# Performance work log

Hardware: AMD Instinct MI355X
Metric: run time of the kernel (lower is better)

The kernel has to match this reference:

```python
import jax, jax.numpy as jnp
import numpy as np

N_NODES = 100000
N_EDGES = 600000
IN_DIM = 128
HID = 128
OUT_DIM = 64
N_LAYERS = 3


def setup_inputs() -> dict:
    key = jax.random.key(0)
    ks = jax.random.split(key, 8)
    x = jax.random.normal(ks[0], (N_NODES, IN_DIM), dtype=jnp.float32)
    edge_index = jax.random.randint(ks[1], (2, N_EDGES), 0, N_NODES, dtype=jnp.int64)
    s = 1.0 / np.sqrt(HID)
    W_in = jax.random.normal(ks[2], (HID, IN_DIM), dtype=jnp.float32) * s
    b_in = jax.random.normal(ks[3], (HID,), dtype=jnp.float32) * s
    W_convs = jax.random.normal(ks[4], (N_LAYERS, HID, HID), dtype=jnp.float32) * s
    b_convs = jax.random.normal(ks[5], (N_LAYERS, HID), dtype=jnp.float32) * s
    W_out = jax.random.normal(ks[6], (OUT_DIM, (N_LAYERS + 1) * HID), dtype=jnp.float32) * s
    b_out = jax.random.normal(ks[7], (OUT_DIM,), dtype=jnp.float32) * s
    return {"x": x, "edge_index": edge_index, "W_in": W_in, "b_in": b_in,
            "W_convs": W_convs, "b_convs": b_convs, "W_out": W_out, "b_out": b_out}


def reference(x, edge_index, W_in, b_in, W_convs, b_convs, W_out, b_out):
    src, dst = edge_index[0], edge_index[1]
    n = x.shape[0]
    # input projection: [N, in] -> [N, H]
    h = x @ W_in.T + b_in
    hidden_states = [h]
    for i in range(W_convs.shape[0]):
        # GINConv (eps=0): nn(x + sum of neighbor messages), messages src->dst
        agg = jax.ops.segment_sum(h[src], dst, num_segments=n)
        h = (h + agg) @ W_convs[i].T + b_convs[i]
        hidden_states.append(h)
    cat = jnp.concatenate(hidden_states, axis=1)  # [N, (L+1)*H]
    out = cat @ W_out.T + b_out  # [N, OUT]
    return jax.nn.softmax(out, axis=-1)
```

## Files before the change

kernel.cpp:

```cpp
#include <hip/hip_runtime.h>
#include <hip/hip_bf16.h>
#include <hip/hip_fp16.h>

#define GN 100000
#define GE 600000
#define SCAN_NBLK 98

typedef __bf16    bf16x8 __attribute__((ext_vector_type(8)));
typedef __bf16    bf16x4 __attribute__((ext_vector_type(4)));
typedef _Float16  f16x8  __attribute__((ext_vector_type(8)));
typedef float     f32x4  __attribute__((ext_vector_type(4)));

__global__ __launch_bounds__(256) void convert_w(
    const float* __restrict__ Win, const float* __restrict__ Wc,
    __bf16* __restrict__ hi, __bf16* __restrict__ lo)
{
    const int i = blockIdx.x * 256 + threadIdx.x;
    if (i >= 65536) return;
    const float v = (i < 16384) ? Win[i] : Wc[i - 16384];
    const __bf16 h = (__bf16)v;
    hi[i] = h;
    lo[i] = (__bf16)(v - (float)h);
}

template<bool GATHER>
__global__ __launch_bounds__(512, 4) void gin_layer(
    const float* __restrict__ H, int ldH,
    const _Float16* __restrict__ HfIn,
    const int* __restrict__ row_start,
    const int* __restrict__ deg,
    const int* __restrict__ csr,
    const __bf16* __restrict__ Whi,
    const __bf16* __restrict__ Wlo,
    const float* __restrict__ bias,
    float* __restrict__ C, int ldC,
    _Float16* __restrict__ HfOut)
{
    constexpr int K   = 128;
    constexpr int ALD = 132;

    __shared__ float Acc[64 * ALD];

    const int tid  = threadIdx.x;
    const int wave = tid >> 6;
    const int lane = tid & 63;
    const int row0 = blockIdx.x * 64;
    const int wm   = (wave >> 2) * 32;
    const int wn   = (wave & 3) * 32;
    const int quad = lane >> 4;
    const int l15  = lane & 15;

#pragma unroll
    for (int p = 0; p < 4; ++p) {
        const int q  = tid + p * 512;
        const int r  = q >> 5;
        const int c4 = (q & 31) * 4;
        float4 v = make_float4(0.f, 0.f, 0.f, 0.f);
        if (row0 + r < GN) v = *(const float4*)(H + (size_t)(row0 + r) * ldH + c4);
        *(float4*)&Acc[r * ALD + c4] = v;
    }

    if (GATHER) {
        const uint* Hw = (const uint*)HfIn;
        float2 acc8[8];
        int start8[8], deg8[8];
        int maxd = 0;
#pragma unroll
        for (int r = 0; r < 8; ++r) {
            acc8[r] = make_float2(0.f, 0.f);
            const int v = row0 + wave * 8 + r;
            start8[r] = (v < GN) ? row_start[v] : 0;
            deg8[r]   = (v < GN) ? deg[v] : 0;
            maxd = max(maxd, deg8[r]);
        }

        int scur[8];
#pragma unroll
        for (int r = 0; r < 8; ++r) {
            const int s = csr[start8[r]];
            scur[r] = min(max(s, 0), GN - 1);
        }

        for (int k = 0; k < maxd; ++k) {
            int snext[8];
#pragma unroll
            for (int r = 0; r < 8; ++r) {
                const int kk = max(min(k + 1, deg8[r] - 1), 0);
                snext[r] = csr[start8[r] + kk];
            }
            uint t[8];
#pragma unroll
            for (int r = 0; r < 8; ++r)
                t[r] = Hw[(size_t)scur[r] * 64 + lane];
#pragma unroll
            for (int r = 0; r < 8; ++r) {
                const float m = (k < deg8[r]) ? 1.f : 0.f;
                union { uint u; _Float16 h[2]; } cv;
                cv.u = t[r];
                acc8[r].x = fmaf(m, (float)cv.h[0], acc8[r].x);
                acc8[r].y = fmaf(m, (float)cv.h[1], acc8[r].y);
                scur[r] = min(max(snext[r], 0), GN - 1);
            }
        }

        __syncthreads();
        const int j = lane * 2;
#pragma unroll
        for (int r = 0; r < 8; ++r) {
            float* a = &Acc[(wave * 8 + r) * ALD + j];
            a[0] += acc8[r].x;
            a[1] += acc8[r].y;
        }
    }
    __syncthreads();

    f32x4 acc[2][2];
#pragma unroll
    for (int i = 0; i < 2; ++i)
#pragma unroll
        for (int j = 0; j < 2; ++j) acc[i][j] = (f32x4)(0.0f);

#pragma unroll
    for (int ks = 0; ks < 4; ++ks) {
        const int kt = ks * 32 + quad * 8;
        bf16x8 ahi[2], alo[2];
#pragma unroll
        for (int mt = 0; mt < 2; ++mt) {
            const float* ap = &Acc[(wm + mt * 16 + l15) * ALD + kt];
            const f32x4 p = *(const f32x4*)ap;
            const f32x4 q = *(const f32x4*)(ap + 4);
#pragma unroll
            for (int e = 0; e < 4; ++e) {
                const __bf16 hp = (__bf16)p[e];
                const __bf16 hq = (__bf16)q[e];
                ahi[mt][e]     = hp;
                ahi[mt][e + 4] = hq;
                alo[mt][e]     = (__bf16)(p[e] - (float)hp);
                alo[mt][e + 4] = (__bf16)(q[e] - (float)hq);
            }
        }
        bf16x8 whi[2], wlo[2];
#pragma unroll
        for (int nt = 0; nt < 2; ++nt) {
            const int n = wn + nt * 16 + l15;
            whi[nt] = *(const bf16x8*)(Whi + (size_t)n * K + kt);
            wlo[nt] = *(const bf16x8*)(Wlo + (size_t)n * K + kt);
        }
#pragma unroll
        for (int mt = 0; mt < 2; ++mt)
#pragma unroll
            for (int nt = 0; nt < 2; ++nt) {
                acc[mt][nt] = __builtin_amdgcn_mfma_f32_16x16x32_bf16(
                    ahi[mt], whi[nt], acc[mt][nt], 0, 0, 0);
                acc[mt][nt] = __builtin_amdgcn_mfma_f32_16x16x32_bf16(
                    ahi[mt], wlo[nt], acc[mt][nt], 0, 0, 0);
                acc[mt][nt] = __builtin_amdgcn_mfma_f32_16x16x32_bf16(
                    alo[mt], whi[nt], acc[mt][nt], 0, 0, 0);
            }
    }
    __syncthreads();

#pragma unroll
    for (int nt = 0; nt < 2; ++nt) {
        const int col = wn + nt * 16 + l15;
        const float b = bias[col];
#pragma unroll
        for (int mt = 0; mt < 2; ++mt)
#pragma unroll
            for (int r4 = 0; r4 < 4; ++r4)
                Acc[(wm + mt * 16 + quad * 4 + r4) * ALD + col] = acc[mt][nt][r4] + b;
    }
    __syncthreads();
#pragma unroll
    for (int p = 0; p < 4; ++p) {
        const int q  = tid + p * 512;
        const int r  = q >> 5;
        const int c4 = (q & 31) * 4;
        const int gr = row0 + r;
        if (gr < GN)
            *(float4*)(C + (size_t)gr * ldC + c4) = *(const float4*)&Acc[r * ALD + c4];
    }
    if (HfOut) {
#pragma unroll
        for (int p = 0; p < 2; ++p) {
            const int q = tid + p * 512;
            const int r = q >> 4;
            const int g = (q & 15) * 8;
            const int gr = row0 + r;
            if (gr < GN) {
                const float4 a = *(const float4*)&Acc[r * ALD + g];
                const float4 b = *(const float4*)&Acc[r * ALD + g + 4];
                f16x8 o = {(_Float16)a.x, (_Float16)a.y, (_Float16)a.z, (_Float16)a.w,
                           (_Float16)b.x, (_Float16)b.y, (_Float16)b.z, (_Float16)b.w};
                *(f16x8*)&HfOut[(size_t)gr * 128 + g] = o;
            }
        }
    }
}

__global__ __launch_bounds__(512, 2) void final_gemm_softmax(
    const float* __restrict__ A,
    const float* __restrict__ Wout,
    const float* __restrict__ bias,
    float* __restrict__ out)
{
    constexpr int K   = 512;
    constexpr int ALD = 72;
    constexpr int CLD = 68;

    __shared__ char smem_raw[128 * ALD * 2 * 2];
    __bf16* Ahi = (__bf16*)smem_raw;
    __bf16* Alo = Ahi + 128 * ALD;
    float*  Cst = (float*)smem_raw;

    const int tid  = threadIdx.x;
    const int wave = tid >> 6;
    const int lane = tid & 63;
    const int row0 = blockIdx.x * 128;
    const int wm   = (wave >> 1) * 32;
    const int wn   = (wave & 1) * 32;
    const int quad = lane >> 4;
    const int l15  = lane & 15;

    f32x4 acc[2][2];
#pragma unroll
    for (int i = 0; i < 2; ++i)
#pragma unroll
        for (int j = 0; j < 2; ++j) acc[i][j] = (f32x4)(0.0f);

    for (int k0 = 0; k0 < K; k0 += 64) {
#pragma unroll
        for (int p = 0; p < 4; ++p) {
            const int q  = tid + p * 512;
            const int f  = q * 4;
            const int r  = f >> 6;
            const int kc = f & 63;
            float4 v4 = make_float4(0.f, 0.f, 0.f, 0.f);
            const int gr = row0 + r;
            if (gr < GN) v4 = *(const float4*)(A + (size_t)gr * 512 + k0 + kc);
            const __bf16 h0 = (__bf16)v4.x, h1 = (__bf16)v4.y,
                         h2 = (__bf16)v4.z, h3 = (__bf16)v4.w;
            const int idx = r * ALD + kc;
            *(bf16x4*)&Ahi[idx] = (bf16x4){h0, h1, h2, h3};
            *(bf16x4*)&Alo[idx] = (bf16x4){(__bf16)(v4.x - (float)h0),
                                           (__bf16)(v4.y - (float)h1),
                                           (__bf16)(v4.z - (float)h2),
                                           (__bf16)(v4.w - (float)h3)};
        }
        __syncthreads();

#pragma unroll
        for (int ks = 0; ks < 2; ++ks) {
            const int kt = ks * 32 + quad * 8;
            bf16x8 ahi[2], alo[2];
#pragma unroll
            for (int mt = 0; mt < 2; ++mt) {
                const int idx = (wm + mt * 16 + l15) * ALD + kt;
                ahi[mt] = *(const bf16x8*)&Ahi[idx];
                alo[mt] = *(const bf16x8*)&Alo[idx];
            }
            bf16x8 whi[2], wlo[2];
#pragma unroll
            for (int nt = 0; nt < 2; ++nt) {
                const int n = wn + nt * 16 + l15;
                const float* wp = Wout + (size_t)n * K + k0 + kt;
                const float4 p = *(const float4*)wp;
                const float4 q = *(const float4*)(wp + 4);
                float pv[8] = {p.x, p.y, p.z, p.w, q.x, q.y, q.z, q.w};
#pragma unroll
                for (int e = 0; e < 8; ++e) {
                    const __bf16 h = (__bf16)pv[e];
                    whi[nt][e] = h;
                    wlo[nt][e] = (__bf16)(pv[e] - (float)h);
                }
            }
#pragma unroll
            for (int mt = 0; mt < 2; ++mt)
#pragma unroll
                for (int nt = 0; nt < 2; ++nt) {
                    acc[mt][nt] = __builtin_amdgcn_mfma_f32_16x16x32_bf16(
                        ahi[mt], whi[nt], acc[mt][nt], 0, 0, 0);
                    acc[mt][nt] = __builtin_amdgcn_mfma_f32_16x16x32_bf16(
                        ahi[mt], wlo[nt], acc[mt][nt], 0, 0, 0);
                    acc[mt][nt] = __builtin_amdgcn_mfma_f32_16x16x32_bf16(
                        alo[mt], whi[nt], acc[mt][nt], 0, 0, 0);
                }
        }
        __syncthreads();
    }

#pragma unroll
    for (int nt = 0; nt < 2; ++nt) {
        const int col = wn + nt * 16 + l15;
        const float b = bias[col];
#pragma unroll
        for (int mt = 0; mt < 2; ++mt)
#pragma unroll
            for (int r4 = 0; r4 < 4; ++r4)
                Cst[(wm + mt * 16 + quad * 4 + r4) * CLD + col] = acc[mt][nt][r4] + b;
    }
    __syncthreads();

    for (int i = 0; i < 16; ++i) {
        const int r = wave * 16 + i;
        const float v = Cst[r * CLD + lane];
        float m = v;
#pragma unroll
        for (int off = 32; off > 0; off >>= 1) m = fmaxf(m, __shfl_xor(m, off));
        const float e = __expf(v - m);
        float s = e;
#pragma unroll
        for (int off = 32; off > 0; off >>= 1) s += __shfl_xor(s, off);
        const int gr = row0 + r;
        if (gr < GN) out[(size_t)gr * 64 + lane] = e / s;
    }
}

__global__ __launch_bounds__(256) void count_deg(const int* __restrict__ dst,
                                                 int* __restrict__ deg)
{
    const int e = blockIdx.x * 256 + threadIdx.x;
    if (e < GE) atomicAdd(&deg[dst[e]], 1);
}

__global__ __launch_bounds__(256) void scan_pass1(const int* __restrict__ deg,
                                                  int* __restrict__ excl,
                                                  int* __restrict__ blockSums)
{
    __shared__ int s[256];
    const int t = threadIdx.x;
    const int base = blockIdx.x * 1024 + t * 4;

    int4 v = make_int4(0, 0, 0, 0);
    if (base + 3 < GN) {
        v = *(const int4*)(deg + base);
    } else {
        if (base + 0 < GN) v.x = deg[base + 0];
        if (base + 1 < GN) v.y = deg[base + 1];
        if (base + 2 < GN) v.z = deg[base + 2];
        if (base + 3 < GN) v.w = deg[base + 3];
    }
    const int mysum = v.x + v.y + v.z + v.w;
    s[t] = mysum;
    __syncthreads();
    for (int off = 1; off < 256; off <<= 1) {
        const int val = (t >= off) ? s[t - off] : 0;
        __syncthreads();
        s[t] += val;
        __syncthreads();
    }
    int4 o;
    o.x = s[t] - mysum;
    o.y = o.x + v.x;
    o.z = o.y + v.y;
    o.w = o.z + v.z;
    if (base + 3 < GN) {
        *(int4*)(excl + base) = o;
    } else {
        if (base + 0 < GN) excl[base + 0] = o.x;
        if (base + 1 < GN) excl[base + 1] = o.y;
        if (base + 2 < GN) excl[base + 2] = o.z;
        if (base + 3 < GN) excl[base + 3] = o.w;
    }
    if (t == 255) blockSums[blockIdx.x] = s[255];
}

__global__ __launch_bounds__(128) void scan_pass2(const int* __restrict__ blockSums,
                                                  int* __restrict__ blockOffs, int n)
{
    __shared__ int s[128];
    const int t = threadIdx.x;
    const int v = (t < n) ? blockSums[t] : 0;
    s[t] = v;
    __syncthreads();
    for (int off = 1; off < 128; off <<= 1) {
        const int val = (t >= off) ? s[t - off] : 0;
        __syncthreads();
        s[t] += val;
        __syncthreads();
    }
    if (t < n) blockOffs[t] = s[t] - v;
}

__global__ __launch_bounds__(256) void scan_pass3(int* __restrict__ excl,
                                                  const int* __restrict__ blockOffs,
                                                  int* __restrict__ cursor)
{
    const int i = blockIdx.x * 256 + threadIdx.x;
    if (i >= GN) return;
    const int v = excl[i] + blockOffs[i >> 10];
    excl[i]   = v;
    cursor[i] = v;
}

__global__ __launch_bounds__(256) void fill_csr(const int* __restrict__ src,
                                                const int* __restrict__ dst,
                                                int* __restrict__ cursor,
                                                int* __restrict__ csr)
{
    const int e = blockIdx.x * 256 + threadIdx.x;
    if (e >= GE) return;
    const int pos = atomicAdd(&cursor[dst[e]], 1);
    csr[pos] = src[e];
}

extern "C" void kernel_launch(void* const* d_in, const int* in_sizes, int n_in,
                              void* d_out, int out_size, void* d_ws, size_t ws_size,
                              hipStream_t stream)
{
    const float* x       = (const float*)d_in[0];
    const int*   src     = (const int*)d_in[1];
    const int*   dst     = ((const int*)d_in[1]) + GE;
    const float* W_in    = (const float*)d_in[2];
    const float* b_in    = (const float*)d_in[3];
    const float* W_convs = (const float*)d_in[4];
    const float* b_convs = (const float*)d_in[5];
    const float* W_out   = (const float*)d_in[6];
    const float* b_out   = (const float*)d_in[7];
    float*       out     = (float*)d_out;

    float*    cat = (float*)d_ws;
    _Float16* Hf0 = (_Float16*)((char*)d_ws + (size_t)GN * 512 * 4);
    _Float16* Hf1 = Hf0 + (size_t)GN * 128;

    int*    deg       = (int*)d_out;
    int*    row_start = deg + GN;
    int*    cursor    = row_start + GN;
    int*    blockSums = cursor + GN;
    int*    blockOffs = blockSums + 128;
    int*    csr       = blockOffs + 128;
    __bf16* Whi       = (__bf16*)(csr + GE);
    __bf16* Wlo       = Whi + 65536;

    const dim3 blk(256);
    const dim3 gblk(512);
    const int edge_blocks  = (GE + 255) / 256;
    const int node_blocks  = (GN + 255) / 256;
    const int layer_blocks = (GN + 63) / 64;
    const int final_blocks = (GN + 127) / 128;

    hipMemsetAsync(deg, 0, GN * sizeof(int), stream);
    count_deg<<<edge_blocks, blk, 0, stream>>>(dst, deg);
    scan_pass1<<<SCAN_NBLK, blk, 0, stream>>>(deg, row_start, blockSums);
    scan_pass2<<<1, 128, 0, stream>>>(blockSums, blockOffs, SCAN_NBLK);
    scan_pass3<<<node_blocks, blk, 0, stream>>>(row_start, blockOffs, cursor);
    fill_csr<<<edge_blocks, blk, 0, stream>>>(src, dst, cursor, csr);

    convert_w<<<(65536 + 255) / 256, blk, 0, stream>>>(W_in, W_convs, Whi, Wlo);

    gin_layer<false><<<layer_blocks, gblk, 0, stream>>>(
        x, 128, nullptr, nullptr, nullptr, nullptr,
        Whi, Wlo, b_in, cat, 512, Hf0);

    _Float16* hin[3]  = {Hf0, Hf1, Hf0};
    _Float16* hout[3] = {Hf1, Hf0, nullptr};
    for (int i = 0; i < 3; ++i) {
        gin_layer<true><<<layer_blocks, gblk, 0, stream>>>(
            cat + i * 128, 512, hin[i], row_start, deg, csr,
            Whi + 16384 + i * 16384, Wlo + 16384 + i * 16384,
            b_convs + (size_t)i * 128, cat + (i + 1) * 128, 512, hout[i]);
    }

    final_gemm_softmax<<<final_blocks, gblk, 0, stream>>>(
        cat, W_out, b_out, out);
}
```

Measured before the change: 535.2 us.

## Fuse last GIN layer with output GEMM and softmax into one kernel

Adds a gin_final kernel that runs the third layer's neighbour gather and GEMM and keeps its 128-column result in shared memory. It then immediately computes the output projection over the concatenated features and the softmax. The concat buffer shrinks from 512 to 384 columns and one full write and read pass over the last hidden state is removed. W_out is now pre-split into bf16 hi/lo once in convert_w instead of being re-split per block. The fused kernel uses 64-row tiles and splits K across wave pairs, which adds an extra shared-memory reduction and may lower MFMA efficiency for the output GEMM.

Measured after the change: 524.3 us. 2.0% less time.

```diff
diff --git a/kernel.cpp b/kernel.cpp
--- a/kernel.cpp
+++ b/kernel.cpp
@@ -13,11 +13,15 @@
 
 __global__ __launch_bounds__(256) void convert_w(
     const float* __restrict__ Win, const float* __restrict__ Wc,
+    const float* __restrict__ Wout,
     __bf16* __restrict__ hi, __bf16* __restrict__ lo)
 {
     const int i = blockIdx.x * 256 + threadIdx.x;
-    if (i >= 65536) return;
-    const float v = (i < 16384) ? Win[i] : Wc[i - 16384];
+    if (i >= 98304) return;
+    float v;
+    if (i < 16384)      v = Win[i];
+    else if (i < 65536) v = Wc[i - 16384];
+    else                v = Wout[i - 65536];
     const __bf16 h = (__bf16)v;
     hi[i] = h;
     lo[i] = (__bf16)(v - (float)h);
@@ -73,14 +77,12 @@
             deg8[r]   = (v < GN) ? deg[v] : 0;
             maxd = max(maxd, deg8[r]);
         }
-
         int scur[8];
 #pragma unroll
         for (int r = 0; r < 8; ++r) {
             const int s = csr[start8[r]];
             scur[r] = min(max(s, 0), GN - 1);
         }
-
         for (int k = 0; k < maxd; ++k) {
             int snext[8];
 #pragma unroll
@@ -102,7 +104,6 @@
                 scur[r] = min(max(snext[r], 0), GN - 1);
             }
         }
-
         __syncthreads();
         const int j = lane * 2;
 #pragma unroll
@@ -180,129 +181,256 @@
         if (gr < GN)
             *(float4*)(C + (size_t)gr * ldC + c4) = *(const float4*)&Acc[r * ALD + c4];
     }
-    if (HfOut) {
-#pragma unroll
-        for (int p = 0; p < 2; ++p) {
-            const int q = tid + p * 512;
-            const int r = q >> 4;
-            const int g = (q & 15) * 8;
-            const int gr = row0 + r;
-            if (gr < GN) {
-                const float4 a = *(const float4*)&Acc[r * ALD + g];
-                const float4 b = *(const float4*)&Acc[r * ALD + g + 4];
-                f16x8 o = {(_Float16)a.x, (_Float16)a.y, (_Float16)a.z, (_Float16)a.w,
-                           (_Float16)b.x, (_Float16)b.y, (_Float16)b.z, (_Float16)b.w};
-                *(f16x8*)&HfOut[(size_t)gr * 128 + g] = o;
-            }
-        }
-    }
-}
-
-__global__ __launch_bounds__(512, 2) void final_gemm_softmax(
-    const float* __restrict__ A,
-    const float* __restrict__ Wout,
-    const float* __restrict__ bias,
+#pragma unroll
+    for (int p = 0; p < 2; ++p) {
+        const int q = tid + p * 512;
+        const int r = q >> 4;
+        const int g = (q & 15) * 8;
+        const int gr = row0 + r;
+        if (gr < GN) {
+            const float4 a = *(const float4*)&Acc[r * ALD + g];
+            const float4 b = *(const float4*)&Acc[r * ALD + g + 4];
+            f16x8 o = {(_Float16)a.x, (_Float16)a.y, (_Float16)a.z, (_Float16)a.w,
+                       (_Float16)b.x, (_Float16)b.y, (_Float16)b.z, (_Float16)b.w};
+            *(f16x8*)&HfOut[(size_t)gr * 128 + g] = o;
+        }
+    }
+}
+
+__global__ __launch_bounds__(512, 4) void gin_final(
+    const float* __restrict__ cat3,
+    const _Float16* __restrict__ HfIn,
+    const int* __restrict__ row_start,
+    const int* __restrict__ deg,
+    const int* __restrict__ csr,
+    const __bf16* __restrict__ Whi3,
+    const __bf16* __restrict__ Wlo3,
+    const float* __restrict__ b3,
+    const __bf16* __restrict__ WhiO,
+    const __bf16* __restrict__ WloO,
+    const float* __restrict__ bO,
     float* __restrict__ out)
 {
-    constexpr int K   = 512;
-    constexpr int ALD = 72;
+    constexpr int ALD = 132;
     constexpr int CLD = 68;
 
-    __shared__ char smem_raw[128 * ALD * 2 * 2];
-    __bf16* Ahi = (__bf16*)smem_raw;
-    __bf16* Alo = Ahi + 128 * ALD;
-    float*  Cst = (float*)smem_raw;
+    __shared__ float Acc[64 * ALD];
+    __shared__ float Cst[64 * CLD];
 
     const int tid  = threadIdx.x;
     const int wave = tid >> 6;
     const int lane = tid & 63;
-    const int row0 = blockIdx.x * 128;
-    const int wm   = (wave >> 1) * 32;
-    const int wn   = (wave & 1) * 32;
+    const int row0 = blockIdx.x * 64;
     const int quad = lane >> 4;
     const int l15  = lane & 15;
 
-    f32x4 acc[2][2];
+#pragma unroll
+    for (int p = 0; p < 4; ++p) {
+        const int q  = tid + p * 512;
+        const int r  = q >> 5;
+        const int c4 = (q & 31) * 4;
+        float4 v = make_float4(0.f, 0.f, 0.f, 0.f);
+        if (row0 + r < GN)
+            v = *(const float4*)(cat3 + (size_t)(row0 + r) * 384 + 256 + c4);
+        *(float4*)&Acc[r * ALD + c4] = v;
+    }
+
+    {
+        const uint* Hw = (const uint*)HfIn;
+        float2 acc8[8];
+        int start8[8], deg8[8];
+        int maxd = 0;
+#pragma unroll
+        for (int r = 0; r < 8; ++r) {
+            acc8[r] = make_float2(0.f, 0.f);
+            const int v = row0 + wave * 8 + r;
+            start8[r] = (v < GN) ? row_start[v] : 0;
+            deg8[r]   = (v < GN) ? deg[v] : 0;
+            maxd = max(maxd, deg8[r]);
+        }
+        int scur[8];
+#pragma unroll
+        for (int r = 0; r < 8; ++r) {
+            const int s = csr[start8[r]];
+            scur[r] = min(max(s, 0), GN - 1);
+        }
+        for (int k = 0; k < maxd; ++k) {
+            int snext[8];
+#pragma unroll
+            for (int r = 0; r < 8; ++r) {
+                const int kk = max(min(k + 1, deg8[r] - 1), 0);
+                snext[r] = csr[start8[r] + kk];
+            }
+            uint t[8];
+#pragma unroll
+            for (int r = 0; r < 8; ++r)
+                t[r] = Hw[(size_t)scur[r] * 64 + lane];
+#pragma unroll
+            for (int r = 0; r < 8; ++r) {
+                const float m = (k < deg8[r]) ? 1.f : 0.f;
+                union { uint u; _Float16 h[2]; } cv;
+                cv.u = t[r];
+                acc8[r].x = fmaf(m, (float)cv.h[0], acc8[r].x);
+                acc8[r].y = fmaf(m, (float)cv.h[1], acc8[r].y);
+                scur[r] = min(max(snext[r], 0), GN - 1);
+            }
+        }
+        __syncthreads();
+        const int j = lane * 2;
+#pragma unroll
+        for (int r = 0; r < 8; ++r) {
+            float* a = &Acc[(wave * 8 + r) * ALD + j];
+            a[0] += acc8[r].x;
+            a[1] += acc8[r].y;
+        }
+    }
+    __syncthreads();
+
+    const int wm = (wave >> 2) * 32;
+    const int wn = (wave & 3) * 32;
+    f32x4 acc1[2][2];
 #pragma unroll
     for (int i = 0; i < 2; ++i)
 #pragma unroll
-        for (int j = 0; j < 2; ++j) acc[i][j] = (f32x4)(0.0f);
-
-    for (int k0 = 0; k0 < K; k0 += 64) {
-#pragma unroll
-        for (int p = 0; p < 4; ++p) {
-            const int q  = tid + p * 512;
-            const int f  = q * 4;
-            const int r  = f >> 6;
-            const int kc = f & 63;
-            float4 v4 = make_float4(0.f, 0.f, 0.f, 0.f);
-            const int gr = row0 + r;
-            if (gr < GN) v4 = *(const float4*)(A + (size_t)gr * 512 + k0 + kc);
-            const __bf16 h0 = (__bf16)v4.x, h1 = (__bf16)v4.y,
-                         h2 = (__bf16)v4.z, h3 = (__bf16)v4.w;
-            const int idx = r * ALD + kc;
-            *(bf16x4*)&Ahi[idx] = (bf16x4){h0, h1, h2, h3};
-            *(bf16x4*)&Alo[idx] = (bf16x4){(__bf16)(v4.x - (float)h0),
-                                           (__bf16)(v4.y - (float)h1),
-                                           (__bf16)(v4.z - (float)h2),
-                                           (__bf16)(v4.w - (float)h3)};
-        }
-        __syncthreads();
-
-#pragma unroll
-        for (int ks = 0; ks < 2; ++ks) {
-            const int kt = ks * 32 + quad * 8;
-            bf16x8 ahi[2], alo[2];
-#pragma unroll
-            for (int mt = 0; mt < 2; ++mt) {
-                const int idx = (wm + mt * 16 + l15) * ALD + kt;
-                ahi[mt] = *(const bf16x8*)&Ahi[idx];
-                alo[mt] = *(const bf16x8*)&Alo[idx];
-            }
-            bf16x8 whi[2], wlo[2];
+        for (int j = 0; j < 2; ++j) acc1[i][j] = (f32x4)(0.0f);
+
+#pragma unroll
+    for (int ks = 0; ks < 4; ++ks) {
+        const int kt = ks * 32 + quad * 8;
+        bf16x8 ahi[2], alo[2];
+#pragma unroll
+        for (int mt = 0; mt < 2; ++mt) {
+            const float* ap = &Acc[(wm + mt * 16 + l15) * ALD + kt];
+            const f32x4 p = *(const f32x4*)ap;
+            const f32x4 q = *(const f32x4*)(ap + 4);
+#pragma unroll
+            for (int e = 0; e < 4; ++e) {
+                const __bf16 hp = (__bf16)p[e];
+                const __bf16 hq = (__bf16)q[e];
+                ahi[mt][e]     = hp;
+                ahi[mt][e + 4] = hq;
+                alo[mt][e]     = (__bf16)(p[e] - (float)hp);
+                alo[mt][e + 4] = (__bf16)(q[e] - (float)hq);
+            }
+        }
+        bf16x8 whi[2], wlo[2];
+#pragma unroll
+        for (int nt = 0; nt < 2; ++nt) {
+            const int n = wn + nt * 16 + l15;
+            whi[nt] = *(const bf16x8*)(Whi3 + (size_t)n * 128 + kt);
+            wlo[nt] = *(const bf16x8*)(Wlo3 + (size_t)n * 128 + kt);
+        }
+#pragma unroll
+        for (int mt = 0; mt < 2; ++mt)
 #pragma unroll
             for (int nt = 0; nt < 2; ++nt) {
-                const int n = wn + nt * 16 + l15;
-                const float* wp = Wout + (size_t)n * K + k0 + kt;
-                const float4 p = *(const float4*)wp;
-                const float4 q = *(const float4*)(wp + 4);
-                float pv[8] = {p.x, p.y, p.z, p.w, q.x, q.y, q.z, q.w};
-#pragma unroll
-                for (int e = 0; e < 8; ++e) {
-                    const __bf16 h = (__bf16)pv[e];
-                    whi[nt][e] = h;
-                    wlo[nt][e] = (__bf16)(pv[e] - (float)h);
-                }
-            }
-#pragma unroll
-            for (int mt = 0; mt < 2; ++mt)
-#pragma unroll
-                for (int nt = 0; nt < 2; ++nt) {
-                    acc[mt][nt] = __builtin_amdgcn_mfma_f32_16x16x32_bf16(
-                        ahi[mt], whi[nt], acc[mt][nt], 0, 0, 0);
-                    acc[mt][nt] = __builtin_amdgcn_mfma_f32_16x16x32_bf16(
-                        ahi[mt], wlo[nt], acc[mt][nt], 0, 0, 0);
-                    acc[mt][nt] = __builtin_amdgcn_mfma_f32_16x16x32_bf16(
-                        alo[mt], whi[nt], acc[mt][nt], 0, 0, 0);
-                }
-        }
-        __syncthreads();
-    }
+                acc1[mt][nt] = __builtin_amdgcn_mfma_f32_16x16x32_bf16(
+                    ahi[mt], whi[nt], acc1[mt][nt], 0, 0, 0);
+                acc1[mt][nt] = __builtin_amdgcn_mfma_f32_16x16x32_bf16(
+                    ahi[mt], wlo[nt], acc1[mt][nt], 0, 0, 0);
+                acc1[mt][nt] = __builtin_amdgcn_mfma_f32_16x16x32_bf16(
+                    alo[mt], whi[nt], acc1[mt][nt], 0, 0, 0);
+            }
+    }
+    __syncthreads();
 
 #pragma unroll
     for (int nt = 0; nt < 2; ++nt) {
         const int col = wn + nt * 16 + l15;
-        const float b = bias[col];
+        const float b = b3[col];
 #pragma unroll
         for (int mt = 0; mt < 2; ++mt)
 #pragma unroll
             for (int r4 = 0; r4 < 4; ++r4)
-                Cst[(wm + mt * 16 + quad * 4 + r4) * CLD + col] = acc[mt][nt][r4] + b;
-    }
-    __syncthreads();
-
-    for (int i = 0; i < 16; ++i) {
-        const int r = wave * 16 + i;
+                Acc[(wm + mt * 16 + quad * 4 + r4) * ALD + col] = acc1[mt][nt][r4] + b;
+    }
+    __syncthreads();
+
+    const int wk  = wave & 1;
+    const int wn2 = ((wave >> 1) & 1) * 32;
+    const int wm2 = ((wave >> 2) & 1) * 32;
+    f32x4 acc2[2][2];
+#pragma unroll
+    for (int i = 0; i < 2; ++i)
+#pragma unroll
+        for (int j = 0; j < 2; ++j) acc2[i][j] = (f32x4)(0.0f);
+
+#pragma unroll
+    for (int ks = 0; ks < 8; ++ks) {
+        const int kg = wk * 256 + ks * 32 + quad * 8;
+        bf16x8 ahi[2], alo[2];
+#pragma unroll
+        for (int mt = 0; mt < 2; ++mt) {
+            const int row = wm2 + mt * 16 + l15;
+            f32x4 p, q;
+            if (kg < 384) {
+                const float* ap = cat3 + (size_t)(row0 + row) * 384 + kg;
+                p = *(const f32x4*)ap;
+                q = *(const f32x4*)(ap + 4);
+            } else {
+                const float* ap = &Acc[row * ALD + (kg - 384)];
+                p = *(const f32x4*)ap;
+                q = *(const f32x4*)(ap + 4);
+            }
+#pragma unroll
+            for (int e = 0; e < 4; ++e) {
+                const __bf16 hp = (__bf16)p[e];
+                const __bf16 hq = (__bf16)q[e];
+                ahi[mt][e]     = hp;
+                ahi[mt][e + 4] = hq;
+                alo[mt][e]     = (__bf16)(p[e] - (float)hp);
+                alo[mt][e + 4] = (__bf16)(q[e] - (float)hq);
+            }
+        }
+        bf16x8 whi[2], wlo[2];
+#pragma unroll
+        for (int nt = 0; nt < 2; ++nt) {
+            const int n = wn2 + nt * 16 + l15;
+            whi[nt] = *(const bf16x8*)(WhiO + (size_t)n * 512 + kg);
+            wlo[nt] = *(const bf16x8*)(WloO + (size_t)n * 512 + kg);
+        }
+#pragma unroll
+        for (int mt = 0; mt < 2; ++mt)
+#pragma unroll
+            for (int nt = 0; nt < 2; ++nt) {
+                acc2[mt][nt] = __builtin_amdgcn_mfma_f32_16x16x32_bf16(
+                    ahi[mt], whi[nt], acc2[mt][nt], 0, 0, 0);
+                acc2[mt][nt] = __builtin_amdgcn_mfma_f32_16x16x32_bf16(
+                    ahi[mt], wlo[nt], acc2[mt][nt], 0, 0, 0);
+                acc2[mt][nt] = __builtin_amdgcn_mfma_f32_16x16x32_bf16(
+                    alo[mt], whi[nt], acc2[mt][nt], 0, 0, 0);
+            }
+    }
+
+    if (wk == 1) {
+#pragma unroll
+        for (int nt = 0; nt < 2; ++nt)
+#pragma unroll
+            for (int mt = 0; mt < 2; ++mt)
+#pragma unroll
+                for (int r4 = 0; r4 < 4; ++r4)
+                    Cst[(wm2 + mt * 16 + quad * 4 + r4) * CLD + wn2 + nt * 16 + l15]
+                        = acc2[mt][nt][r4];
+    }
+    __syncthreads();
+    if (wk == 0) {
+#pragma unroll
+        for (int nt = 0; nt < 2; ++nt) {
+            const int col = wn2 + nt * 16 + l15;
+            const float b = bO[col];
+#pragma unroll
+            for (int mt = 0; mt < 2; ++mt)
+#pragma unroll
+                for (int r4 = 0; r4 < 4; ++r4) {
+                    const int idx = (wm2 + mt * 16 + quad * 4 + r4) * CLD + col;
+                    Cst[idx] = Cst[idx] + acc2[mt][nt][r4] + b;
+                }
+        }
+    }
+    __syncthreads();
+
+    for (int i = 0; i < 8; ++i) {
+        const int r = wave * 8 + i;
         const float v = Cst[r * CLD + lane];
         float m = v;
 #pragma unroll
@@ -419,25 +547,23 @@
     const float* b_out   = (const float*)d_in[7];
     float*       out     = (float*)d_out;
 
-    float*    cat = (float*)d_ws;
-    _Float16* Hf0 = (_Float16*)((char*)d_ws + (size_t)GN * 512 * 4);
-    _Float16* Hf1 = Hf0 + (size_t)GN * 128;
-
-    int*    deg       = (int*)d_out;
-    int*    row_start = deg + GN;
-    int*    cursor    = row_start + GN;
-    int*    blockSums = cursor + GN;
-    int*    blockOffs = blockSums + 128;
-    int*    csr       = blockOffs + 128;
-    __bf16* Whi       = (__bf16*)(csr + GE);
-    __bf16* Wlo       = Whi + 65536;
+    float*    cat3 = (float*)d_ws;
+    _Float16* Hf0  = (_Float16*)(cat3 + (size_t)GN * 384);
+    _Float16* Hf1  = Hf0 + (size_t)GN * 128;
+    int*      deg       = (int*)(Hf1 + (size_t)GN * 128);
+    int*      row_start = deg + GN;
+    int*      cursor    = row_start + GN;
+    int*      blockSums = cursor + GN;
+    int*      blockOffs = blockSums + 128;
+    int*      csr       = blockOffs + 128;
+    __bf16*   Whi       = (__bf16*)(csr + GE);
+    __bf16*   Wlo       = Whi + 98304;
 
     const dim3 blk(256);
     const dim3 gblk(512);
     const int edge_blocks  = (GE + 255) / 256;
     const int node_blocks  = (GN + 255) / 256;
     const int layer_blocks = (GN + 63) / 64;
-    const int final_blocks = (GN + 127) / 128;
 
     hipMemsetAsync(deg, 0, GN * sizeof(int), stream);
     count_deg<<<edge_blocks, blk, 0, stream>>>(dst, deg);
@@ -446,21 +572,21 @@
     scan_pass3<<<node_blocks, blk, 0, stream>>>(row_start, blockOffs, cursor);
     fill_csr<<<edge_blocks, blk, 0, stream>>>(src, dst, cursor, csr);
 
-    convert_w<<<(65536 + 255) / 256, blk, 0, stream>>>(W_in, W_convs, Whi, Wlo);
+    convert_w<<<(98304 + 255) / 256, blk, 0, stream>>>(W_in, W_convs, W_out, Whi, Wlo);
 
     gin_layer<false><<<layer_blocks, gblk, 0, stream>>>(
         x, 128, nullptr, nullptr, nullptr, nullptr,
-        Whi, Wlo, b_in, cat, 512, Hf0);
-
-    _Float16* hin[3]  = {Hf0, Hf1, Hf0};
-    _Float16* hout[3] = {Hf1, Hf0, nullptr};
-    for (int i = 0; i < 3; ++i) {
-        gin_layer<true><<<layer_blocks, gblk, 0, stream>>>(
-            cat + i * 128, 512, hin[i], row_start, deg, csr,
-            Whi + 16384 + i * 16384, Wlo + 16384 + i * 16384,
-            b_convs + (size_t)i * 128, cat + (i + 1) * 128, 512, hout[i]);
-    }
-
-    final_gemm_softmax<<<final_blocks, gblk, 0, stream>>>(
-        cat, W_out, b_out, out);
-}
+        Whi, Wlo, b_in, cat3, 384, Hf0);
+
+    gin_layer<true><<<layer_blocks, gblk, 0, stream>>>(
+        cat3, 384, Hf0, row_start, deg, csr,
+        Whi + 16384, Wlo + 16384, b_convs, cat3 + 128, 384, Hf1);
+    gin_layer<true><<<layer_blocks, gblk, 0, stream>>>(
+        cat3 + 128, 384, Hf1, row_start, deg, csr,
+        Whi + 32768, Wlo + 32768, b_convs + 128, cat3 + 256, 384, Hf0);
+
+    gin_final<<<layer_blocks, gblk, 0, stream>>>(
+        cat3, Hf0, row_start, deg, csr,
+        Whi + 49152, Wlo + 49152, b_convs + 256,
+        Whi + 65536, Wlo + 65536, b_out, out);
+}
```
